# Optimization experiments

Measured on AMD Instinct MI355X. Metric: run time of the kernel, lower is better.

The kernel has to match this reference:

```python
import jax, jax.numpy as jnp
import numpy as np

CHANNELS = 512
NUM_HEADS = 8


def setup_inputs() -> dict:
    key = jax.random.key(0)
    ks = jax.random.split(key, 5)
    c = CHANNELS
    x = jax.random.normal(ks[0], (8, c, 32, 32), dtype=jnp.float32)
    # nn.Linear(channels, 3*channels) weight is (out, in); keep torch layout
    w_qkv = jax.random.normal(ks[1], (3 * c, c), dtype=jnp.float32) / np.sqrt(c)
    b_qkv = jax.random.normal(ks[2], (3 * c,), dtype=jnp.float32) * 0.01
    w_o = jax.random.normal(ks[3], (c, c), dtype=jnp.float32) / np.sqrt(c)
    b_o = jax.random.normal(ks[4], (c,), dtype=jnp.float32) * 0.01
    return {"x": x, "w_qkv": w_qkv, "b_qkv": b_qkv, "w_o": w_o, "b_o": b_o}


def reference(x, w_qkv, b_qkv, w_o, b_o):
    b, c, h, w = x.shape
    nh = NUM_HEADS
    hd = c // nh
    # b c h w -> b (h w) c
    xs = jnp.transpose(x.reshape(b, c, h * w), (0, 2, 1))  # [b, s, c]
    qkv = xs @ w_qkv.T + b_qkv                              # [b, s, 3c]
    q, k, v = qkv[..., :c], qkv[..., c:2 * c], qkv[..., 2 * c:]
    s = h * w
    q = q.reshape(b, s, nh, hd).transpose(0, 2, 1, 3)       # [b, nh, s, hd]
    k = k.reshape(b, s, nh, hd).transpose(0, 2, 1, 3)
    v = v.reshape(b, s, nh, hd).transpose(0, 2, 1, 3)
    scores = jnp.einsum('bnqd,bnkd->bnqk', q, k) / np.sqrt(hd).astype(np.float32)
    probs = jax.nn.softmax(scores, axis=-1)                 # [b, nh, s, s]
    av = jnp.einsum('bnqk,bnkd->bqnd', probs, v).reshape(b, s, c)
    out = av @ w_o.T + b_o                                  # [b, s, c]
    # b (h w) c -> b c h w
    return jnp.transpose(out, (0, 2, 1)).reshape(b, c, h, w)
```

## Files before the change

kernel.cpp:

```cpp
#include <hip/hip_runtime.h>
#include <cstddef>
#include <cstdint>

#define CH 512
#define SEQ 1024
#define NH 8
#define HD 64

typedef unsigned short u16;
typedef __attribute__((ext_vector_type(8))) short bf16x8;
typedef __attribute__((ext_vector_type(4))) float f32x4;
typedef __attribute__((ext_vector_type(4))) unsigned short u16x4;

__device__ __forceinline__ u16 f2bf(float f) {
  unsigned u = __float_as_uint(f);
  u += 0x7fffu + ((u >> 16) & 1u);
  return (u16)(u >> 16);
}
__device__ __forceinline__ float bf2f(u16 h) {
  return __uint_as_float(((unsigned)h) << 16);
}

__device__ __forceinline__ void gld16(void* lds, const void* g) {
  __builtin_amdgcn_global_load_lds(
      (const __attribute__((address_space(1))) unsigned int*)g,
      (__attribute__((address_space(3))) unsigned int*)lds, 16, 0, 0);
}

__device__ __forceinline__ f32x4 mfma16(bf16x8 a, bf16x8 b, f32x4 c) {
  return __builtin_amdgcn_mfma_f32_16x16x32_bf16(a, b, c, 0, 0, 0);
}

__global__ __launch_bounds__(256) void split_plain(
    const float* __restrict__ in, u16* __restrict__ hi, u16* __restrict__ lo, int n4)
{
  int i = blockIdx.x * 256 + threadIdx.x;
  if (i < n4) {
    float4 v = ((const float4*)in)[i];
    float vv0 = v.x, vv1 = v.y, vv2 = v.z, vv3 = v.w;
    u16x4 h, l;
    h[0] = f2bf(vv0); l[0] = f2bf(vv0 - bf2f(h[0]));
    h[1] = f2bf(vv1); l[1] = f2bf(vv1 - bf2f(h[1]));
    h[2] = f2bf(vv2); l[2] = f2bf(vv2 - bf2f(h[2]));
    h[3] = f2bf(vv3); l[3] = f2bf(vv3 - bf2f(h[3]));
    ((u16x4*)hi)[i] = h;
    ((u16x4*)lo)[i] = l;
  }
}

__global__ __launch_bounds__(256) void transpose_split(
    const float* __restrict__ x, u16* __restrict__ xh, u16* __restrict__ xl)
{
  __shared__ float tile[64][65];
  const int s0 = blockIdx.x * 64, c0 = blockIdx.y * 64, bz = blockIdx.z;
  const int t = threadIdx.x;
  #pragma unroll
  for (int p = 0; p < 16; ++p) {
    int i = p * 256 + t;
    int cl = i >> 6, sl = i & 63;
    tile[cl][sl] = x[((size_t)bz * CH + c0 + cl) * SEQ + s0 + sl];
  }
  __syncthreads();
  #pragma unroll
  for (int p = 0; p < 16; ++p) {
    int i = p * 256 + t;
    int sl = i >> 6, cl = i & 63;
    float v = tile[cl][sl];
    u16 h = f2bf(v);
    size_t idx = ((size_t)bz * SEQ + s0 + sl) * CH + c0 + cl;
    xh[idx] = h;
    xl[idx] = f2bf(v - bf2f(h));
  }
}

template<int MODE>
__global__ __launch_bounds__(256, 2) void gemm_hilo(
    const u16* __restrict__ Ah, const u16* __restrict__ Al,
    const u16* __restrict__ BTh, const u16* __restrict__ BTl,
    const float* __restrict__ bias,
    void* __restrict__ o0, void* __restrict__ o1, void* __restrict__ o2,
    void* __restrict__ o3, void* __restrict__ o4)
{
  const int bx = blockIdx.x, by = blockIdx.y, bz = blockIdx.z;
  const int m0 = by * 128, n0 = bx * 128;
  const char* Ahc = (const char*)Ah;
  const char* Alc = (const char*)Al;
  const char* Bhc = (const char*)BTh + (size_t)bz * SEQ * CH * 2;
  const char* Blc = (const char*)BTl + (size_t)bz * SEQ * CH * 2;

  __shared__ __align__(16) u16 As[128 * 64];
  __shared__ __align__(16) u16 Bs[128 * 64];

  const int t = threadIdx.x, w = t >> 6, lane = t & 63;
  const int lr = lane & 15, lg = lane >> 4;
  const int wr = w >> 1, wc = w & 1;

  f32x4 acc[4][4];
  #pragma unroll
  for (int i = 0; i < 4; ++i)
    #pragma unroll
    for (int j = 0; j < 4; ++j) acc[i][j] = (f32x4){0.f, 0.f, 0.f, 0.f};

  for (int k0 = 0; k0 < CH; k0 += 32) {
    __syncthreads();
    #pragma unroll
    for (int p = 0; p < 4; ++p) {
      const int ldsoff = p * 4096 + w * 1024 + lane * 16;
      const int m = ldsoff >> 7;
      const int W = ldsoff & 127;
      const int Wp = W ^ ((m & 7) << 4);
      const char* src = (Wp < 64 ? Ahc : Alc) + ((size_t)(m0 + m) * CH + k0) * 2 + (Wp & 63);
      gld16((char*)As + p * 4096 + w * 1024, src);
    }
    #pragma unroll
    for (int p = 0; p < 4; ++p) {
      const int ldsoff = p * 4096 + w * 1024 + lane * 16;
      const int n = ldsoff >> 7;
      const int W = ldsoff & 127;
      const int Wp = W ^ ((n & 7) << 4);
      const char* src = (Wp < 64 ? Bhc : Blc) + ((size_t)(n0 + n) * CH + k0) * 2 + (Wp & 63);
      gld16((char*)Bs + p * 4096 + w * 1024, src);
    }
    __syncthreads();

    bf16x8 Afh[4], Afl[4], Bfh[4], Bfl[4];
    #pragma unroll
    for (int mi = 0; mi < 4; ++mi) {
      const int m = wr * 64 + mi * 16 + lr;
      const int swz = (m & 7) << 4;
      Afh[mi] = *(const bf16x8*)((const char*)As + m * 128 + ((lg * 16) ^ swz));
      Afl[mi] = *(const bf16x8*)((const char*)As + m * 128 + ((64 + lg * 16) ^ swz));
    }
    #pragma unroll
    for (int ni = 0; ni < 4; ++ni) {
      const int n = wc * 64 + ni * 16 + lr;
      const int swz = (n & 7) << 4;
      Bfh[ni] = *(const bf16x8*)((const char*)Bs + n * 128 + ((lg * 16) ^ swz));
      Bfl[ni] = *(const bf16x8*)((const char*)Bs + n * 128 + ((64 + lg * 16) ^ swz));
    }
    #pragma unroll
    for (int mi = 0; mi < 4; ++mi) {
      #pragma unroll
      for (int ni = 0; ni < 4; ++ni) {
        acc[mi][ni] = mfma16(Afh[mi], Bfh[ni], acc[mi][ni]);
        acc[mi][ni] = mfma16(Afh[mi], Bfl[ni], acc[mi][ni]);
        acc[mi][ni] = mfma16(Afl[mi], Bfh[ni], acc[mi][ni]);
      }
    }
  }

  if constexpr (MODE == 0) {
    float* Out = (float*)o0 + (size_t)bz * CH * SEQ;
    #pragma unroll
    for (int mi = 0; mi < 4; ++mi) {
      const int mb = m0 + wr * 64 + mi * 16 + lg * 4;
      #pragma unroll
      for (int r = 0; r < 4; ++r) {
        const float bv = bias[mb + r];
        #pragma unroll
        for (int ni = 0; ni < 4; ++ni) {
          const int n = n0 + wc * 64 + ni * 16 + lr;
          Out[(size_t)(mb + r) * SEQ + n] = acc[mi][ni][r] + bv;
        }
      }
    }
  } else {
    u16* qh = (u16*)o0; u16* ql = (u16*)o1;
    u16* kh = (u16*)o2; u16* kl = (u16*)o3;
    u16* vh = (u16*)o4;
    #pragma unroll
    for (int mi = 0; mi < 4; ++mi) {
      const int mb = m0 + wr * 64 + mi * 16 + lg * 4;
      const int sec = mb >> 9;
      const int h = (mb >> 6) & 7;
      const int d = mb & 63;
      const size_t bh = (size_t)bz * NH + h;
      const float b0 = bias[mb + 0], b1 = bias[mb + 1], b2 = bias[mb + 2], b3 = bias[mb + 3];
      #pragma unroll
      for (int ni = 0; ni < 4; ++ni) {
        const int n = n0 + wc * 64 + ni * 16 + lr;
        const float c0 = acc[mi][ni][0] + b0;
        const float c1 = acc[mi][ni][1] + b1;
        const float c2 = acc[mi][ni][2] + b2;
        const float c3 = acc[mi][ni][3] + b3;
        if (sec == 2) {
          u16* dst = vh + (bh * HD + d) * SEQ + n;
          dst[0 * SEQ] = f2bf(c0);
          dst[1 * SEQ] = f2bf(c1);
          dst[2 * SEQ] = f2bf(c2);
          dst[3 * SEQ] = f2bf(c3);
        } else {
          u16* dsth = (sec == 0 ? qh : kh) + (bh * SEQ + n) * HD + d;
          u16* dstl = (sec == 0 ? ql : kl) + (bh * SEQ + n) * HD + d;
          u16x4 hv, lv;
          hv[0] = f2bf(c0); lv[0] = f2bf(c0 - bf2f(hv[0]));
          hv[1] = f2bf(c1); lv[1] = f2bf(c1 - bf2f(hv[1]));
          hv[2] = f2bf(c2); lv[2] = f2bf(c2 - bf2f(hv[2]));
          hv[3] = f2bf(c3); lv[3] = f2bf(c3 - bf2f(hv[3]));
          *(u16x4*)dsth = hv;
          *(u16x4*)dstl = lv;
        }
      }
    }
  }
}

__global__ __launch_bounds__(256, 2) void attn_mfma(
    const u16* __restrict__ q_h, const u16* __restrict__ q_l,
    const u16* __restrict__ k_h, const u16* __restrict__ k_l,
    const u16* __restrict__ v_h,
    u16* __restrict__ av_h, u16* __restrict__ av_l)
{
  const int qt = blockIdx.x, hh = blockIdx.y, bz = blockIdx.z;
  const int bhead = bz * NH + hh;
  const int s0 = qt * 64;
  const int t = threadIdx.x, w = t >> 6, lane = t & 63;
  const int lr = lane & 15, lg = lane >> 4;

  __shared__ __align__(16) u16 Kh_s[64 * 64];
  __shared__ __align__(16) u16 Kl_s[64 * 64];
  __shared__ __align__(16) u16 Vs_s[64 * 64];
  __shared__ __align__(16) u16 Ps_s[4 * 16 * 64];

  bf16x8 QAh[2], QAl[2];
  {
    const size_t qrow = (size_t)bhead * SEQ + s0 + w * 16 + lr;
    #pragma unroll
    for (int ks = 0; ks < 2; ++ks) {
      QAh[ks] = *(const bf16x8*)((const char*)q_h + qrow * 128 + ks * 64 + lg * 16);
      QAl[ks] = *(const bf16x8*)((const char*)q_l + qrow * 128 + ks * 64 + lg * 16);
    }
  }

  float mrow[4], lsum[4];
  f32x4 oacc[4];
  #pragma unroll
  for (int r = 0; r < 4; ++r) { mrow[r] = -1e30f; lsum[r] = 0.f; }
  #pragma unroll
  for (int ni = 0; ni < 4; ++ni) oacc[ni] = (f32x4){0.f, 0.f, 0.f, 0.f};

  for (int kt = 0; kt < 16; ++kt) {
    __syncthreads();
    {
      const size_t kbase = (size_t)bhead * SEQ + kt * 64;
      #pragma unroll
      for (int p = 0; p < 2; ++p) {
        const int ldsoff = p * 4096 + w * 1024 + lane * 16;
        const int r = ldsoff >> 7;
        const int W = ldsoff & 127;
        const int Wp = W ^ ((r & 7) << 4);
        gld16((char*)Kh_s + p * 4096 + w * 1024, (const char*)k_h + (kbase + r) * 128 + Wp);
        gld16((char*)Kl_s + p * 4096 + w * 1024, (const char*)k_l + (kbase + r) * 128 + Wp);
        gld16((char*)Vs_s + p * 4096 + w * 1024,
              (const char*)v_h + ((size_t)bhead * HD + r) * 2048 + kt * 128 + Wp);
      }
    }
    __syncthreads();

    f32x4 sc[4];
    #pragma unroll
    for (int ni = 0; ni < 4; ++ni) sc[ni] = (f32x4){0.f, 0.f, 0.f, 0.f};
    #pragma unroll
    for (int ks = 0; ks < 2; ++ks) {
      #pragma unroll
      for (int ni = 0; ni < 4; ++ni) {
        const int kj = ni * 16 + lr;
        const int off = (ks * 64 + lg * 16) ^ ((kj & 7) << 4);
        bf16x8 kbh = *(const bf16x8*)((const char*)Kh_s + kj * 128 + off);
        bf16x8 kbl = *(const bf16x8*)((const char*)Kl_s + kj * 128 + off);
        sc[ni] = mfma16(QAh[ks], kbh, sc[ni]);
        sc[ni] = mfma16(QAh[ks], kbl, sc[ni]);
        sc[ni] = mfma16(QAl[ks], kbh, sc[ni]);
      }
    }
    #pragma unroll
    for (int ni = 0; ni < 4; ++ni)
      #pragma unroll
      for (int r = 0; r < 4; ++r) sc[ni][r] *= 0.125f;

    float tm[4], rs[4], al[4];
    #pragma unroll
    for (int r = 0; r < 4; ++r)
      tm[r] = fmaxf(fmaxf(sc[0][r], sc[1][r]), fmaxf(sc[2][r], sc[3][r]));
    #pragma unroll
    for (int off = 1; off < 16; off <<= 1) {
      #pragma unroll
      for (int r = 0; r < 4; ++r) tm[r] = fmaxf(tm[r], __shfl_xor(tm[r], off));
    }
    #pragma unroll
    for (int r = 0; r < 4; ++r) {
      const float mn = fmaxf(mrow[r], tm[r]);
      al[r] = __expf(mrow[r] - mn);
      mrow[r] = mn;
      rs[r] = 0.f;
    }
    #pragma unroll
    for (int ni = 0; ni < 4; ++ni) {
      #pragma unroll
      for (int r = 0; r < 4; ++r) {
        const float pf = __expf(sc[ni][r] - mrow[r]);
        rs[r] += pf;
        const int qi = lg * 4 + r;
        const int col = ni * 16 + lr;
        *(u16*)((char*)Ps_s + w * 2048 + qi * 128 + ((col * 2) ^ ((qi & 7) << 4))) = f2bf(pf);
      }
    }
    #pragma unroll
    for (int off = 1; off < 16; off <<= 1) {
      #pragma unroll
      for (int r = 0; r < 4; ++r) rs[r] += __shfl_xor(rs[r], off);
    }
    #pragma unroll
    for (int r = 0; r < 4; ++r) lsum[r] = lsum[r] * al[r] + rs[r];
    #pragma unroll
    for (int ni = 0; ni < 4; ++ni)
      #pragma unroll
      for (int r = 0; r < 4; ++r) oacc[ni][r] *= al[r];

    #pragma unroll
    for (int ks = 0; ks < 2; ++ks) {
      const int off0 = ks * 64 + lg * 16;
      bf16x8 pa = *(const bf16x8*)((const char*)Ps_s + w * 2048 + lr * 128 + (off0 ^ ((lr & 7) << 4)));
      #pragma unroll
      for (int ni = 0; ni < 4; ++ni) {
        const int d = ni * 16 + lr;
        bf16x8 vb = *(const bf16x8*)((const char*)Vs_s + d * 128 + (off0 ^ ((d & 7) << 4)));
        oacc[ni] = mfma16(pa, vb, oacc[ni]);
      }
    }
  }

  #pragma unroll
  for (int r = 0; r < 4; ++r) {
    const float inv = 1.f / lsum[r];
    const int s = s0 + w * 16 + lg * 4 + r;
    #pragma unroll
    for (int ni = 0; ni < 4; ++ni) {
      const int c = hh * HD + ni * 16 + lr;
      const size_t idx = ((size_t)bz * SEQ + s) * CH + c;
      const float v = oacc[ni][r] * inv;
      const u16 hb = f2bf(v);
      av_h[idx] = hb;
      av_l[idx] = f2bf(v - bf2f(hb));
    }
  }
}

extern "C" void kernel_launch(void* const* d_in, const int* in_sizes, int n_in,
                              void* d_out, int out_size, void* d_ws, size_t ws_size,
                              hipStream_t stream) {
  const float* x     = (const float*)d_in[0];
  const float* w_qkv = (const float*)d_in[1];
  const float* b_qkv = (const float*)d_in[2];
  const float* w_o   = (const float*)d_in[3];
  const float* b_o   = (const float*)d_in[4];
  float* out = (float*)d_out;

  char* ws = (char*)d_ws;
  const size_t SZ = (size_t)8 * SEQ * CH * 2;
  u16* xt_h = (u16*)(ws + 0 * SZ);
  u16* xt_l = (u16*)(ws + 1 * SZ);
  u16* q_h  = (u16*)(ws + 2 * SZ);
  u16* q_l  = (u16*)(ws + 3 * SZ);
  u16* k_h  = (u16*)(ws + 4 * SZ);
  u16* k_l  = (u16*)(ws + 5 * SZ);
  u16* v_h  = (u16*)(ws + 6 * SZ);
  u16* wqkv_h = (u16*)(ws + 7 * SZ);
  u16* wqkv_l = wqkv_h + (size_t)1536 * 512;
  u16* wo_h   = wqkv_l + (size_t)1536 * 512;
  u16* wo_l   = wo_h + (size_t)512 * 512;

  split_plain<<<768, 256, 0, stream>>>(w_qkv, wqkv_h, wqkv_l, (1536 * 512) / 4);
  split_plain<<<256, 256, 0, stream>>>(w_o, wo_h, wo_l, (512 * 512) / 4);
  transpose_split<<<dim3(16, 8, 8), 256, 0, stream>>>(x, xt_h, xt_l);

  gemm_hilo<1><<<dim3(8, 12, 8), 256, 0, stream>>>(
      wqkv_h, wqkv_l, xt_h, xt_l, b_qkv,
      (void*)q_h, (void*)q_l, (void*)k_h, (void*)k_l, (void*)v_h);

  attn_mfma<<<dim3(16, 8, 8), 256, 0, stream>>>(
      q_h, q_l, k_h, k_l, v_h, xt_h, xt_l);

  gemm_hilo<0><<<dim3(8, 4, 8), 256, 0, stream>>>(
      wo_h, wo_l, xt_h, xt_l, b_o,
      (void*)out, nullptr, nullptr, nullptr, nullptr);
}
```

Before: 215.1 us.

## Load K/V tiles directly from global into registers, drop LDS staging and barriers

```diff
diff --git a/kernel.cpp b/kernel.cpp
--- a/kernel.cpp
+++ b/kernel.cpp
@@ -217,9 +217,6 @@
   const int t = threadIdx.x, w = t >> 6, lane = t & 63;
   const int lr = lane & 15, lg = lane >> 4;
 
-  __shared__ __align__(16) u16 Kh_s[64 * 64];
-  __shared__ __align__(16) u16 Kl_s[64 * 64];
-  __shared__ __align__(16) u16 Vs_s[64 * 64];
   __shared__ __align__(16) u16 Ps_s[4 * 16 * 64];
 
   bf16x8 QAh[2], QAl[2];
@@ -232,6 +229,12 @@
     }
   }
 
+  const char* Khb = (const char*)k_h + (size_t)bhead * SEQ * 128;
+  const char* Klb = (const char*)k_l + (size_t)bhead * SEQ * 128;
+  const char* Vbb = (const char*)v_h + (size_t)bhead * HD * 2048;
+
+  const float SCL = 0.1803368801111204f;
+
   float mrow[4], lsum[4];
   f32x4 oacc[4];
   #pragma unroll
@@ -240,43 +243,31 @@
   for (int ni = 0; ni < 4; ++ni) oacc[ni] = (f32x4){0.f, 0.f, 0.f, 0.f};
 
   for (int kt = 0; kt < 16; ++kt) {
-    __syncthreads();
-    {
-      const size_t kbase = (size_t)bhead * SEQ + kt * 64;
-      #pragma unroll
-      for (int p = 0; p < 2; ++p) {
-        const int ldsoff = p * 4096 + w * 1024 + lane * 16;
-        const int r = ldsoff >> 7;
-        const int W = ldsoff & 127;
-        const int Wp = W ^ ((r & 7) << 4);
-        gld16((char*)Kh_s + p * 4096 + w * 1024, (const char*)k_h + (kbase + r) * 128 + Wp);
-        gld16((char*)Kl_s + p * 4096 + w * 1024, (const char*)k_l + (kbase + r) * 128 + Wp);
-        gld16((char*)Vs_s + p * 4096 + w * 1024,
-              (const char*)v_h + ((size_t)bhead * HD + r) * 2048 + kt * 128 + Wp);
-      }
-    }
-    __syncthreads();
-
     f32x4 sc[4];
     #pragma unroll
     for (int ni = 0; ni < 4; ++ni) sc[ni] = (f32x4){0.f, 0.f, 0.f, 0.f};
     #pragma unroll
     for (int ks = 0; ks < 2; ++ks) {
-      #pragma unroll
-      for (int ni = 0; ni < 4; ++ni) {
-        const int kj = ni * 16 + lr;
-        const int off = (ks * 64 + lg * 16) ^ ((kj & 7) << 4);
-        bf16x8 kbh = *(const bf16x8*)((const char*)Kh_s + kj * 128 + off);
-        bf16x8 kbl = *(const bf16x8*)((const char*)Kl_s + kj * 128 + off);
-        sc[ni] = mfma16(QAh[ks], kbh, sc[ni]);
-        sc[ni] = mfma16(QAh[ks], kbl, sc[ni]);
-        sc[ni] = mfma16(QAl[ks], kbh, sc[ni]);
-      }
+      bf16x8 kbh[4], kbl[4];
+      #pragma unroll
+      for (int ni = 0; ni < 4; ++ni) {
+        const int kj = kt * 64 + ni * 16 + lr;
+        kbh[ni] = *(const bf16x8*)(Khb + (size_t)kj * 128 + ks * 64 + lg * 16);
+        kbl[ni] = *(const bf16x8*)(Klb + (size_t)kj * 128 + ks * 64 + lg * 16);
+      }
+      __builtin_amdgcn_s_setprio(1);
+      #pragma unroll
+      for (int ni = 0; ni < 4; ++ni) {
+        sc[ni] = mfma16(QAh[ks], kbh[ni], sc[ni]);
+        sc[ni] = mfma16(QAh[ks], kbl[ni], sc[ni]);
+        sc[ni] = mfma16(QAl[ks], kbh[ni], sc[ni]);
+      }
+      __builtin_amdgcn_s_setprio(0);
     }
     #pragma unroll
     for (int ni = 0; ni < 4; ++ni)
       #pragma unroll
-      for (int r = 0; r < 4; ++r) sc[ni][r] *= 0.125f;
+      for (int r = 0; r < 4; ++r) sc[ni][r] *= SCL;
 
     float tm[4], rs[4], al[4];
     #pragma unroll
@@ -290,7 +281,7 @@
     #pragma unroll
     for (int r = 0; r < 4; ++r) {
       const float mn = fmaxf(mrow[r], tm[r]);
-      al[r] = __expf(mrow[r] - mn);
+      al[r] = exp2f(mrow[r] - mn);
       mrow[r] = mn;
       rs[r] = 0.f;
     }
@@ -298,7 +289,7 @@
     for (int ni = 0; ni < 4; ++ni) {
       #pragma unroll
       for (int r = 0; r < 4; ++r) {
-        const float pf = __expf(sc[ni][r] - mrow[r]);
+        const float pf = exp2f(sc[ni][r] - mrow[r]);
         rs[r] += pf;
         const int qi = lg * 4 + r;
         const int col = ni * 16 + lr;
@@ -321,12 +312,16 @@
     for (int ks = 0; ks < 2; ++ks) {
       const int off0 = ks * 64 + lg * 16;
       bf16x8 pa = *(const bf16x8*)((const char*)Ps_s + w * 2048 + lr * 128 + (off0 ^ ((lr & 7) << 4)));
+      bf16x8 vb[4];
       #pragma unroll
       for (int ni = 0; ni < 4; ++ni) {
         const int d = ni * 16 + lr;
-        bf16x8 vb = *(const bf16x8*)((const char*)Vs_s + d * 128 + (off0 ^ ((d & 7) << 4)));
-        oacc[ni] = mfma16(pa, vb, oacc[ni]);
-      }
+        vb[ni] = *(const bf16x8*)(Vbb + (size_t)d * 2048 + kt * 128 + ks * 64 + lg * 16);
+      }
+      __builtin_amdgcn_s_setprio(1);
+      #pragma unroll
+      for (int ni = 0; ni < 4; ++ni) oacc[ni] = mfma16(pa, vb[ni], oacc[ni]);
+      __builtin_amdgcn_s_setprio(0);
     }
   }
 
```

Result: slower. 319.7 us (+48.6%).
